# Performance work log

Hardware: AMD Instinct MI355X
Metric: run time of the kernel (lower is better)

The kernel has to match this reference:

```python
import jax, jax.numpy as jnp
import numpy as np


def setup_inputs() -> dict:
    key = jax.random.key(0)
    ks = jax.random.split(key, 8)
    B, H, W, C = 4, 64, 64, 256
    Ck = C // 8  # key/query channels
    x = jax.random.normal(ks[0], (B, H, W, C), dtype=jnp.float32)
    Wf = jax.random.normal(ks[1], (C, Ck), dtype=jnp.float32) * (1.0 / np.sqrt(C))
    Wg = jax.random.normal(ks[2], (C, Ck), dtype=jnp.float32) * (1.0 / np.sqrt(C))
    Wh = jax.random.normal(ks[3], (C, C), dtype=jnp.float32) * (1.0 / np.sqrt(C))
    bf = jnp.zeros((Ck,), dtype=jnp.float32)
    bg = jnp.zeros((Ck,), dtype=jnp.float32)
    bh = jnp.zeros((C,), dtype=jnp.float32)
    gamma = jax.random.normal(ks[4], (), dtype=jnp.float32) * 0.1
    return {"x": x, "Wf": Wf, "bf": bf, "Wg": Wg, "bg": bg, "Wh": Wh, "bh": bh, "gamma": gamma}


def reference(x, Wf, bf, Wg, bg, Wh, bh, gamma):
    B, H, W, C = x.shape
    N = H * W
    # 1x1 convs == per-pixel matmuls over channel dim
    f = jnp.einsum('bhwc,ck->bhwk', x, Wf) + bf  # [B,H,W,C/8]
    g = jnp.einsum('bhwc,ck->bhwk', x, Wg) + bg  # [B,H,W,C/8]
    h = jnp.einsum('bhwc,cd->bhwd', x, Wh) + bh  # [B,H,W,C]
    f_flat = f.reshape(B, N, -1)
    g_flat = g.reshape(B, N, -1)
    h_flat = h.reshape(B, N, C)
    # s[b,i,j] = <g_i, f_j>   (query = g, key = f, as in the TF code)
    s = jnp.einsum('bik,bjk->bij', g_flat, f_flat)  # [B,N,N]
    b = jax.nn.softmax(s, axis=-1)
    o = jnp.einsum('bij,bjd->bid', b, h_flat)  # [B,N,C]
    y = gamma * o.reshape(B, H, W, C) + x
    return y
```

## Files before the change

### kernel.cpp

```cpp
#include <hip/hip_runtime.h>
#include <hip/hip_bf16.h>
#include <math.h>


typedef __bf16 bf16x8 __attribute__((ext_vector_type(8)));
typedef __bf16 bf16x4 __attribute__((ext_vector_type(4)));
typedef float f32x4 __attribute__((ext_vector_type(4)));

#define NPIX 4096
#define CDIM 256
#define CK   32

__device__ __forceinline__ void gload_lds16(const void* g, void* l) {
    __builtin_amdgcn_global_load_lds(
        (const __attribute__((address_space(1))) unsigned int*)g,
        (__attribute__((address_space(3))) unsigned int*)l, 16, 0, 0);
}

__global__ __launch_bounds__(256) void prep_wtf(
    const float* __restrict__ Wf, const float* __restrict__ Wg,
    const float* __restrict__ Wh, __bf16* __restrict__ WTf)
{
    const int ct = blockIdx.x;
    for (int i = threadIdx.x; i < 16 * 256; i += 256) {
        const int l15 = i >> 8;
        const int k = i & 255;
        const int c = ct * 16 + l15;
        float v;
        if (c < 32)      v = Wf[k * 32 + c];
        else if (c < 64) v = Wg[k * 32 + (c - 32)];
        else             v = Wh[k * 256 + (c - 64)];
        WTf[((size_t)(ct * 8 + (k >> 5)) * 16 + l15) * 32 + (k & 31)] = (__bf16)v;
    }
}

__global__ __launch_bounds__(256, 4) void proj_mfma(
    const float* __restrict__ x, const __bf16* __restrict__ WTf,
    const float* __restrict__ bf_, const float* __restrict__ bg_,
    const float* __restrict__ bh_,
    __bf16* __restrict__ fbuf, __bf16* __restrict__ gbuf,
    __bf16* __restrict__ hT)
{
    __shared__ __bf16 xs[16 * 256];

    const int t = threadIdx.x;
    const int rowbase = blockIdx.x * 16;

    #pragma unroll
    for (int i = 0; i < 4; ++i) {
        const int flat = i * 1024 + t * 4;
        const int row = flat >> 8, col = flat & 255;
        const float4 xv = *(const float4*)&x[(size_t)rowbase * 256 + flat];
        const int sc = col ^ ((row & 7) << 3);
        *(bf16x4*)&xs[row * 256 + sc] =
            (bf16x4){(__bf16)xv.x, (__bf16)xv.y, (__bf16)xv.z, (__bf16)xv.w};
    }
    __syncthreads();

    const int wv = t >> 6, lane = t & 63, l15 = lane & 15, lhi = lane >> 4;

    const f32x4 zero4 = {0.f, 0.f, 0.f, 0.f};
    f32x4 acc[5];
    #pragma unroll
    for (int i = 0; i < 5; ++i) acc[i] = zero4;

    for (int kk = 0; kk < 8; ++kk) {
        const int col = (kk * 32 + lhi * 8) ^ ((l15 & 7) << 3);
        const bf16x8 xfrag = *(const bf16x8*)&xs[l15 * 256 + col];
        if (wv == 0) {
            #pragma unroll
            for (int i = 0; i < 4; ++i) {
                const bf16x8 w = *(const bf16x8*)&WTf[((size_t)(i * 8 + kk) * 16 + l15) * 32 + lhi * 8];
                acc[i] = __builtin_amdgcn_mfma_f32_16x16x32_bf16(xfrag, w, acc[i], 0, 0, 0);
            }
            const bf16x8 w = *(const bf16x8*)&WTf[((size_t)(4 * 8 + kk) * 16 + l15) * 32 + lhi * 8];
            acc[4] = __builtin_amdgcn_mfma_f32_16x16x32_bf16(w, xfrag, acc[4], 0, 0, 0);
        } else {
            #pragma unroll
            for (int i = 0; i < 5; ++i) {
                const int ctg = 4 + (wv - 1) * 5 + i + 1;
                const bf16x8 w = *(const bf16x8*)&WTf[((size_t)(ctg * 8 + kk) * 16 + l15) * 32 + lhi * 8];
                acc[i] = __builtin_amdgcn_mfma_f32_16x16x32_bf16(w, xfrag, acc[i], 0, 0, 0);
            }
        }
    }

    const int b = rowbase >> 12;
    const int n = (rowbase & 4095) + l15;
    if (wv == 0) {
        #pragma unroll
        for (int i = 0; i < 2; ++i) {
            const float bia = bf_[i * 16 + l15];
            #pragma unroll
            for (int r = 0; r < 4; ++r)
                fbuf[(size_t)(rowbase + lhi * 4 + r) * CK + i * 16 + l15] =
                    (__bf16)(acc[i][r] + bia);
        }
        #pragma unroll
        for (int i = 0; i < 2; ++i) {
            const float bia = bg_[i * 16 + l15];
            #pragma unroll
            for (int r = 0; r < 4; ++r)
                gbuf[(size_t)(rowbase + lhi * 4 + r) * CK + i * 16 + l15] =
                    (__bf16)(acc[i + 2][r] + bia);
        }
        #pragma unroll
        for (int r = 0; r < 4; ++r) {
            const int d = lhi * 4 + r;
            hT[((size_t)b * CDIM + d) * NPIX + n] = (__bf16)(acc[4][r] + bh_[d]);
        }
    } else {
        #pragma unroll
        for (int i = 0; i < 5; ++i) {
            const int dt = (wv - 1) * 5 + i + 1;
            #pragma unroll
            for (int r = 0; r < 4; ++r) {
                const int d = dt * 16 + lhi * 4 + r;
                hT[((size_t)b * CDIM + d) * NPIX + n] = (__bf16)(acc[i][r] + bh_[d]);
            }
        }
    }
}

#define ATTN_BODY(T, HU, HL)                                                        \
{                                                                                   \
    const int cb_ = (T) & 1;                                                        \
    if (wv < 4) {                                                                   \
        const f32x4 m30 = {-30.f, -30.f, -30.f, -30.f};                             \
        f32x4 s[4];                                                                 \
        _Pragma("unroll")                                                           \
        for (int cb = 0; cb < 4; ++cb) {                                            \
            const int r = cb * 16 + l15;                                            \
            const bf16x8 fr = *(const bf16x8*)                                      \
                &fs[cb_][r][(lhi ^ (r & 3) ^ ((r >> 2) & 3)) * 8];                  \
            s[cb] = __builtin_amdgcn_mfma_f32_16x16x32_bf16(ga, fr, m30, 0, 0, 0);  \
        }                                                                           \
        _Pragma("unroll")                                                           \
        for (int cb = 0; cb < 4; ++cb) {                                            \
            _Pragma("unroll")                                                       \
            for (int r = 0; r < 4; ++r) {                                           \
                const float p = __expf(s[cb][r]);                                   \
                lsum[r] += p;                                                       \
                pbuf[cb_][wv * 16 + lhi * 4 + r][cb * 16 + l15] = (__bf16)p;        \
            }                                                                       \
        }                                                                           \
        if ((T) < 63)                                                               \
            gload_lds16(fsrc_ + (size_t)((T) + 1) * 64 * CK,                        \
                        &fs[cb_ ^ 1][wv * 16][0]);                                  \
    }                                                                               \
    __syncthreads();                                                                \
    if ((T) < 63) {                                                                 \
        const size_t kvn = (size_t)((T) + 1) * 64;                                  \
        _Pragma("unroll")                                                           \
        for (int dt = 0; dt < 2; ++dt)                                              \
            _Pragma("unroll")                                                       \
            for (int kh = 0; kh < 2; ++kh)                                          \
                HL[dt * 2 + kh] = *(const bf16x8*)                                  \
                    (hp + (size_t)dt * 16 * NPIX + kvn + kh * 32);                  \
    }                                                                               \
    __builtin_amdgcn_s_setprio(1);                                                  \
    _Pragma("unroll")                                                               \
    for (int rt = 0; rt < 4; ++rt) {                                                \
        const bf16x8 pa0 = *(const bf16x8*)&pbuf[cb_][rt * 16 + l15][lhi * 8];      \
        const bf16x8 pa1 = *(const bf16x8*)&pbuf[cb_][rt * 16 + l15][32 + lhi * 8]; \
        _Pragma("unroll")                                                           \
        for (int dt = 0; dt < 2; ++dt) {                                            \
            O_[rt][dt] = __builtin_amdgcn_mfma_f32_16x16x32_bf16(                   \
                pa0, HU[dt * 2 + 0], O_[rt][dt], 0, 0, 0);                          \
            O_[rt][dt] = __builtin_amdgcn_mfma_f32_16x16x32_bf16(                   \
                pa1, HU[dt * 2 + 1], O_[rt][dt], 0, 0, 0);                          \
        }                                                                           \
    }                                                                               \
    __builtin_amdgcn_s_setprio(0);                                                  \
}

__global__ __launch_bounds__(512, 2) void attn_kernel(
    const __bf16* __restrict__ fbuf, const __bf16* __restrict__ gbuf,
    const __bf16* __restrict__ hT, const float* __restrict__ x,
    const float* __restrict__ gamma_p, float* __restrict__ out)
{
    __shared__ __bf16 pbuf[2][64][72];
    __shared__ __bf16 fs[2][64][32];
    __shared__ float lbuf[64];

    const int t = threadIdx.x;
    const int lane = t & 63;
    const int wv = t >> 6;
    const int l15 = lane & 15;
    const int lhi = lane >> 4;

    const int xcd = blockIdx.x & 7;
    const int b = xcd >> 1;
    const int qt = ((blockIdx.x >> 3) << 1) + (xcd & 1);
    const int q0 = qt * 64;

    const __bf16* hb = hT + (size_t)b * CDIM * NPIX;
    const __bf16* fbp = fbuf + (size_t)b * NPIX * CK;

    const __bf16* hp = hb + (size_t)(wv * 32 + l15) * NPIX + lhi * 8;

    bf16x8 ga = {};
    if (wv < 4)
        ga = *(const bf16x8*)&gbuf[((size_t)b * NPIX + q0 + wv * 16 + l15) * CK + lhi * 8];
    const int frow = lane >> 2;
    const __bf16* fsrc_ = fbp + (size_t)(wv * 16 + frow) * CK
                              + ((lane & 3) ^ (frow & 3) ^ ((frow >> 2) & 3)) * 8;

    const f32x4 zero4 = {0.f, 0.f, 0.f, 0.f};
    f32x4 O_[4][2];
    #pragma unroll
    for (int i = 0; i < 4; ++i) { O_[i][0] = zero4; O_[i][1] = zero4; }
    float lsum[4] = {0.f, 0.f, 0.f, 0.f};

    bf16x8 hA[4], hB[4];

    if (wv < 4) gload_lds16(fsrc_, &fs[0][wv * 16][0]);
    #pragma unroll
    for (int dt = 0; dt < 2; ++dt)
        #pragma unroll
        for (int kh = 0; kh < 2; ++kh)
            hA[dt * 2 + kh] = *(const bf16x8*)(hp + (size_t)dt * 16 * NPIX + kh * 32);
    __syncthreads();

    for (int it = 0; it < 32; ++it) {
        ATTN_BODY(2 * it,     hA, hB);
        ATTN_BODY(2 * it + 1, hB, hA);
    }

    if (wv < 4) {
        #pragma unroll
        for (int r = 0; r < 4; ++r) {
            lsum[r] += __shfl_xor(lsum[r], 1, 64);
            lsum[r] += __shfl_xor(lsum[r], 2, 64);
            lsum[r] += __shfl_xor(lsum[r], 4, 64);
            lsum[r] += __shfl_xor(lsum[r], 8, 64);
        }
        if (l15 == 0) {
            #pragma unroll
            for (int r = 0; r < 4; ++r)
                lbuf[wv * 16 + lhi * 4 + r] = lsum[r];
        }
    }
    __syncthreads();

    const float gm = gamma_p[0];
    #pragma unroll
    for (int rt = 0; rt < 4; ++rt) {
        #pragma unroll
        for (int rr = 0; rr < 4; ++rr) {
            const int row = rt * 16 + lhi * 4 + rr;
            const float rl = gm / lbuf[row];
            const size_t base = ((size_t)b * NPIX + q0 + row) * CDIM + wv * 32;
            #pragma unroll
            for (int dt = 0; dt < 2; ++dt) {
                const size_t idx = base + dt * 16 + l15;
                out[idx] = fmaf(rl, O_[rt][dt][rr], x[idx]);
            }
        }
    }
}

extern "C" void kernel_launch(void* const* d_in, const int* in_sizes, int n_in,
                              void* d_out, int out_size, void* d_ws, size_t ws_size,
                              hipStream_t stream)
{
    const float* x     = (const float*)d_in[0];
    const float* Wf    = (const float*)d_in[1];
    const float* bf    = (const float*)d_in[2];
    const float* Wg    = (const float*)d_in[3];
    const float* bg    = (const float*)d_in[4];
    const float* Wh    = (const float*)d_in[5];
    const float* bh    = (const float*)d_in[6];
    const float* gamma = (const float*)d_in[7];
    float* out = (float*)d_out;

    __bf16* fbuf = (__bf16*)d_ws;
    __bf16* gbuf = fbuf + (size_t)4 * NPIX * CK;
    __bf16* hT   = gbuf + (size_t)4 * NPIX * CK;
    __bf16* WTf  = hT + (size_t)4 * CDIM * NPIX;

    prep_wtf<<<20, 256, 0, stream>>>(Wf, Wg, Wh, WTf);
    proj_mfma<<<1024, 256, 0, stream>>>(x, WTf, bf, bg, bh, fbuf, gbuf, hT);
    attn_kernel<<<256, 512, 0, stream>>>(fbuf, gbuf, hT, x, gamma, out);
}
```

Baseline: 178.2 us.

## Rework projection tiling and attention kernel with register-held K and permlane P packing

The projection kernel now handles 64 rows per 512-thread block, with a split of waves between the f/g and h outputs so weight fragments are reused across row blocks. It also uses packed bf16 conversion. The attention kernel drops the LDS staging of f and loads K fragments straight into double-buffered registers. Softmax probabilities are packed with permlane swaps into a compact LDS layout, and the PV work is rebalanced so the four score waves take fewer output columns. prep_wtf is also parallelized over more blocks. This aims to cut LDS traffic and barrier stalls and to balance work across waves, at the cost of higher register pressure and a 1-block occupancy bound.

```diff
diff --git a/kernel.cpp b/kernel.cpp
--- a/kernel.cpp
+++ b/kernel.cpp
@@ -4,183 +4,222 @@
 
 
 typedef __bf16 bf16x8 __attribute__((ext_vector_type(8)));
-typedef __bf16 bf16x4 __attribute__((ext_vector_type(4)));
 typedef float f32x4 __attribute__((ext_vector_type(4)));
 
 #define NPIX 4096
 #define CDIM 256
 #define CK   32
 
-__device__ __forceinline__ void gload_lds16(const void* g, void* l) {
-    __builtin_amdgcn_global_load_lds(
-        (const __attribute__((address_space(1))) unsigned int*)g,
-        (__attribute__((address_space(3))) unsigned int*)l, 16, 0, 0);
+union U128 { unsigned int d[4]; uint4 u4; bf16x8 v; };
+
+__device__ __forceinline__ unsigned int cvtpk(float lo, float hi) {
+    unsigned int r;
+    asm("v_cvt_pk_bf16_f32 %0, %1, %2" : "=v"(r) : "v"(lo), "v"(hi));
+    return r;
 }
 
 __global__ __launch_bounds__(256) void prep_wtf(
     const float* __restrict__ Wf, const float* __restrict__ Wg,
     const float* __restrict__ Wh, __bf16* __restrict__ WTf)
 {
-    const int ct = blockIdx.x;
-    for (int i = threadIdx.x; i < 16 * 256; i += 256) {
-        const int l15 = i >> 8;
-        const int k = i & 255;
-        const int c = ct * 16 + l15;
-        float v;
-        if (c < 32)      v = Wf[k * 32 + c];
-        else if (c < 64) v = Wg[k * 32 + (c - 32)];
-        else             v = Wh[k * 256 + (c - 64)];
-        WTf[((size_t)(ct * 8 + (k >> 5)) * 16 + l15) * 32 + (k & 31)] = (__bf16)v;
-    }
-}
-
-__global__ __launch_bounds__(256, 4) void proj_mfma(
+    const int k = blockIdx.x;
+    const int c = threadIdx.x;
+    const int kk = k >> 5, kj = k & 31;
+    {
+        const float v = Wh[k * 256 + c];
+        const int ct = 4 + (c >> 4), l15 = c & 15;
+        WTf[((size_t)(ct * 8 + kk) * 16 + l15) * 32 + kj] = (__bf16)v;
+    }
+    if (c < 32) {
+        const float v = Wf[k * 32 + c];
+        const int ct = c >> 4, l15 = c & 15;
+        WTf[((size_t)(ct * 8 + kk) * 16 + l15) * 32 + kj] = (__bf16)v;
+    } else if (c < 64) {
+        const int cc = c - 32;
+        const float v = Wg[k * 32 + cc];
+        const int ct = 2 + (cc >> 4), l15 = cc & 15;
+        WTf[((size_t)(ct * 8 + kk) * 16 + l15) * 32 + kj] = (__bf16)v;
+    }
+}
+
+__global__ __launch_bounds__(512, 1) void proj_mfma(
     const float* __restrict__ x, const __bf16* __restrict__ WTf,
     const float* __restrict__ bf_, const float* __restrict__ bg_,
     const float* __restrict__ bh_,
     __bf16* __restrict__ fbuf, __bf16* __restrict__ gbuf,
     __bf16* __restrict__ hT)
 {
-    __shared__ __bf16 xs[16 * 256];
+    __shared__ __bf16 xs[64 * 256];
 
     const int t = threadIdx.x;
-    const int rowbase = blockIdx.x * 16;
+    const int rowbase = blockIdx.x * 64;
 
     #pragma unroll
-    for (int i = 0; i < 4; ++i) {
-        const int flat = i * 1024 + t * 4;
+    for (int i = 0; i < 8; ++i) {
+        const int flat = i * 2048 + t * 4;
         const int row = flat >> 8, col = flat & 255;
         const float4 xv = *(const float4*)&x[(size_t)rowbase * 256 + flat];
-        const int sc = col ^ ((row & 7) << 3);
-        *(bf16x4*)&xs[row * 256 + sc] =
-            (bf16x4){(__bf16)xv.x, (__bf16)xv.y, (__bf16)xv.z, (__bf16)xv.w};
+        const unsigned int d0 = cvtpk(xv.x, xv.y);
+        const unsigned int d1 = cvtpk(xv.z, xv.w);
+        const int s = (col >> 3) ^ (row & 7);
+        uint2 w; w.x = d0; w.y = d1;
+        *(uint2*)&xs[row * 256 + s * 8 + (col & 7)] = w;
     }
     __syncthreads();
 
     const int wv = t >> 6, lane = t & 63, l15 = lane & 15, lhi = lane >> 4;
-
-    const f32x4 zero4 = {0.f, 0.f, 0.f, 0.f};
-    f32x4 acc[5];
-    #pragma unroll
-    for (int i = 0; i < 5; ++i) acc[i] = zero4;
-
-    for (int kk = 0; kk < 8; ++kk) {
-        const int col = (kk * 32 + lhi * 8) ^ ((l15 & 7) << 3);
-        const bf16x8 xfrag = *(const bf16x8*)&xs[l15 * 256 + col];
-        if (wv == 0) {
-            #pragma unroll
-            for (int i = 0; i < 4; ++i) {
-                const bf16x8 w = *(const bf16x8*)&WTf[((size_t)(i * 8 + kk) * 16 + l15) * 32 + lhi * 8];
-                acc[i] = __builtin_amdgcn_mfma_f32_16x16x32_bf16(xfrag, w, acc[i], 0, 0, 0);
-            }
-            const bf16x8 w = *(const bf16x8*)&WTf[((size_t)(4 * 8 + kk) * 16 + l15) * 32 + lhi * 8];
-            acc[4] = __builtin_amdgcn_mfma_f32_16x16x32_bf16(w, xfrag, acc[4], 0, 0, 0);
-        } else {
-            #pragma unroll
-            for (int i = 0; i < 5; ++i) {
-                const int ctg = 4 + (wv - 1) * 5 + i + 1;
-                const bf16x8 w = *(const bf16x8*)&WTf[((size_t)(ctg * 8 + kk) * 16 + l15) * 32 + lhi * 8];
-                acc[i] = __builtin_amdgcn_mfma_f32_16x16x32_bf16(w, xfrag, acc[i], 0, 0, 0);
-            }
-        }
-    }
-
     const int b = rowbase >> 12;
-    const int n = (rowbase & 4095) + l15;
-    if (wv == 0) {
-        #pragma unroll
-        for (int i = 0; i < 2; ++i) {
-            const float bia = bf_[i * 16 + l15];
-            #pragma unroll
-            for (int r = 0; r < 4; ++r)
-                fbuf[(size_t)(rowbase + lhi * 4 + r) * CK + i * 16 + l15] =
-                    (__bf16)(acc[i][r] + bia);
-        }
-        #pragma unroll
-        for (int i = 0; i < 2; ++i) {
-            const float bia = bg_[i * 16 + l15];
-            #pragma unroll
-            for (int r = 0; r < 4; ++r)
-                gbuf[(size_t)(rowbase + lhi * 4 + r) * CK + i * 16 + l15] =
-                    (__bf16)(acc[i + 2][r] + bia);
-        }
-        #pragma unroll
-        for (int r = 0; r < 4; ++r) {
-            const int d = lhi * 4 + r;
-            hT[((size_t)b * CDIM + d) * NPIX + n] = (__bf16)(acc[4][r] + bh_[d]);
+    const int nloc = rowbase & 4095;
+
+    if (wv < 2) {
+        const int rb0 = wv * 2;
+        f32x4 acc[4][2];
+        #pragma unroll
+        for (int c = 0; c < 4; ++c)
+            #pragma unroll
+            for (int rb = 0; rb < 2; ++rb) acc[c][rb] = (f32x4){0.f, 0.f, 0.f, 0.f};
+        #pragma unroll
+        for (int kk = 0; kk < 8; ++kk) {
+            bf16x8 xf[2];
+            #pragma unroll
+            for (int rb = 0; rb < 2; ++rb) {
+                const int row = (rb0 + rb) * 16 + l15;
+                xf[rb] = *(const bf16x8*)&xs[row * 256 + (((kk * 4 + lhi) ^ (row & 7)) * 8)];
+            }
+            #pragma unroll
+            for (int c = 0; c < 4; ++c) {
+                const bf16x8 w = *(const bf16x8*)&WTf[((size_t)(c * 8 + kk) * 16 + l15) * 32 + lhi * 8];
+                acc[c][0] = __builtin_amdgcn_mfma_f32_16x16x32_bf16(xf[0], w, acc[c][0], 0, 0, 0);
+                acc[c][1] = __builtin_amdgcn_mfma_f32_16x16x32_bf16(xf[1], w, acc[c][1], 0, 0, 0);
+            }
+        }
+        #pragma unroll
+        for (int c = 0; c < 4; ++c) {
+            const float bia = (c < 2) ? bf_[c * 16 + l15] : bg_[(c - 2) * 16 + l15];
+            __bf16* dst = (c < 2) ? fbuf : gbuf;
+            const int ch = (c & 1) * 16 + l15;
+            #pragma unroll
+            for (int rb = 0; rb < 2; ++rb)
+                #pragma unroll
+                for (int r = 0; r < 4; ++r)
+                    dst[(size_t)(rowbase + (rb0 + rb) * 16 + lhi * 4 + r) * CK + ch] =
+                        (__bf16)(acc[c][rb][r] + bia);
         }
     } else {
-        #pragma unroll
-        for (int i = 0; i < 5; ++i) {
-            const int dt = (wv - 1) * 5 + i + 1;
-            #pragma unroll
-            for (int r = 0; r < 4; ++r) {
-                const int d = dt * 16 + lhi * 4 + r;
-                hT[((size_t)b * CDIM + d) * NPIX + n] = (__bf16)(acc[i][r] + bh_[d]);
-            }
-        }
-    }
-}
-
-#define ATTN_BODY(T, HU, HL)                                                        \
-{                                                                                   \
-    const int cb_ = (T) & 1;                                                        \
+        const int nct = (wv < 6) ? 3 : 2;
+        const int ct0 = (wv < 6) ? (wv - 2) * 3 : 12 + (wv - 6) * 2;
+        f32x4 acc[3][4];
+        #pragma unroll
+        for (int c = 0; c < 3; ++c)
+            #pragma unroll
+            for (int rb = 0; rb < 4; ++rb) acc[c][rb] = (f32x4){0.f, 0.f, 0.f, 0.f};
+        #pragma unroll
+        for (int kk = 0; kk < 8; ++kk) {
+            bf16x8 xf[4];
+            #pragma unroll
+            for (int rb = 0; rb < 4; ++rb) {
+                const int row = rb * 16 + l15;
+                xf[rb] = *(const bf16x8*)&xs[row * 256 + (((kk * 4 + lhi) ^ (row & 7)) * 8)];
+            }
+            #pragma unroll
+            for (int c = 0; c < 3; ++c) {
+                if (c < nct) {
+                    const bf16x8 w = *(const bf16x8*)
+                        &WTf[((size_t)((4 + ct0 + c) * 8 + kk) * 16 + l15) * 32 + lhi * 8];
+                    #pragma unroll
+                    for (int rb = 0; rb < 4; ++rb)
+                        acc[c][rb] = __builtin_amdgcn_mfma_f32_16x16x32_bf16(w, xf[rb], acc[c][rb], 0, 0, 0);
+                }
+            }
+        }
+        #pragma unroll
+        for (int c = 0; c < 3; ++c) {
+            if (c < nct) {
+                #pragma unroll
+                for (int r = 0; r < 4; ++r) {
+                    const int ch = (ct0 + c) * 16 + lhi * 4 + r;
+                    const float bia = bh_[ch];
+                    #pragma unroll
+                    for (int rb = 0; rb < 4; ++rb)
+                        hT[((size_t)b * CDIM + ch) * NPIX + nloc + rb * 16 + l15] =
+                            (__bf16)(acc[c][rb][r] + bia);
+                }
+            }
+        }
+    }
+}
+
+#define PL32(a, b) asm("v_permlane32_swap_b32 %0, %1" : "+v"(a), "+v"(b))
+#define PL16(a, b) asm("v_permlane16_swap_b32 %0, %1" : "+v"(a), "+v"(b))
+
+#define ATTN_TILE(KV, PB, FC, FN, HC, HN)                                           \
+do {                                                                                \
     if (wv < 4) {                                                                   \
         const f32x4 m30 = {-30.f, -30.f, -30.f, -30.f};                             \
-        f32x4 s[4];                                                                 \
-        _Pragma("unroll")                                                           \
-        for (int cb = 0; cb < 4; ++cb) {                                            \
-            const int r = cb * 16 + l15;                                            \
-            const bf16x8 fr = *(const bf16x8*)                                      \
-                &fs[cb_][r][(lhi ^ (r & 3) ^ ((r >> 2) & 3)) * 8];                  \
-            s[cb] = __builtin_amdgcn_mfma_f32_16x16x32_bf16(ga, fr, m30, 0, 0, 0);  \
+        f32x4 s0 = __builtin_amdgcn_mfma_f32_16x16x32_bf16(FC[0], ga, m30, 0, 0, 0);\
+        f32x4 s1 = __builtin_amdgcn_mfma_f32_16x16x32_bf16(FC[1], ga, m30, 0, 0, 0);\
+        f32x4 s2 = __builtin_amdgcn_mfma_f32_16x16x32_bf16(FC[2], ga, m30, 0, 0, 0);\
+        f32x4 s3 = __builtin_amdgcn_mfma_f32_16x16x32_bf16(FC[3], ga, m30, 0, 0, 0);\
+        {                                                 \
+            const size_t ko = (size_t)((KV) + 64) * CK;                             \
+            FN[0] = *(const bf16x8*)(fp + ko);                                      \
+            FN[1] = *(const bf16x8*)(fp + ko + 16 * CK);                            \
+            FN[2] = *(const bf16x8*)(fp + ko + 32 * CK);                            \
+            FN[3] = *(const bf16x8*)(fp + ko + 48 * CK);                            \
         }                                                                           \
-        _Pragma("unroll")                                                           \
-        for (int cb = 0; cb < 4; ++cb) {                                            \
-            _Pragma("unroll")                                                       \
-            for (int r = 0; r < 4; ++r) {                                           \
-                const float p = __expf(s[cb][r]);                                   \
-                lsum[r] += p;                                                       \
-                pbuf[cb_][wv * 16 + lhi * 4 + r][cb * 16 + l15] = (__bf16)p;        \
-            }                                                                       \
-        }                                                                           \
-        if ((T) < 63)                                                               \
-            gload_lds16(fsrc_ + (size_t)((T) + 1) * 64 * CK,                        \
-                        &fs[cb_ ^ 1][wv * 16][0]);                                  \
+        float p0 = __expf(s0[0]), p1 = __expf(s0[1]), p2 = __expf(s0[2]), p3 = __expf(s0[3]); \
+        float p4 = __expf(s1[0]), p5 = __expf(s1[1]), p6 = __expf(s1[2]), p7 = __expf(s1[3]); \
+        float p8 = __expf(s2[0]), p9 = __expf(s2[1]), pa_ = __expf(s2[2]), pb_ = __expf(s2[3]); \
+        float pc_ = __expf(s3[0]), pd_ = __expf(s3[1]), pe_ = __expf(s3[2]), pf_ = __expf(s3[3]); \
+        lsum += ((p0 + p1) + (p2 + p3)) + ((p4 + p5) + (p6 + p7))                   \
+              + ((p8 + p9) + (pa_ + pb_)) + ((pc_ + pd_) + (pe_ + pf_));            \
+        unsigned int u0 = cvtpk(p0, p1), u1 = cvtpk(p2, p3);                        \
+        unsigned int u2 = cvtpk(p4, p5), u3 = cvtpk(p6, p7);                        \
+        unsigned int u4 = cvtpk(p8, p9), u5 = cvtpk(pa_, pb_);                      \
+        unsigned int u6 = cvtpk(pc_, pd_), u7 = cvtpk(pe_, pf_);                    \
+        PL32(u0, u2); PL32(u1, u3); PL32(u4, u6); PL32(u5, u7);                     \
+        PL16(u0, u2); PL16(u1, u3); PL16(u4, u6); PL16(u5, u7);                     \
+        uint4 w0; w0.x = u0; w0.y = u1; w0.z = u2; w0.w = u3;                       \
+        uint4 w1; w1.x = u4; w1.y = u5; w1.z = u6; w1.w = u7;                       \
+        pbuf[PB][wv * 2 + 0][lane] = w0;                                            \
+        pbuf[PB][wv * 2 + 1][lane] = w1;                                            \
     }                                                                               \
     __syncthreads();                                                                \
-    if ((T) < 63) {                                                                 \
-        const size_t kvn = (size_t)((T) + 1) * 64;                                  \
-        _Pragma("unroll")                                                           \
-        for (int dt = 0; dt < 2; ++dt)                                              \
-            _Pragma("unroll")                                                       \
-            for (int kh = 0; kh < 2; ++kh)                                          \
-                HL[dt * 2 + kh] = *(const bf16x8*)                                  \
-                    (hp + (size_t)dt * 16 * NPIX + kvn + kh * 32);                  \
+    {                                                     \
+        const size_t kn = (size_t)((KV) + 64);                                      \
+        HN[0] = *(const bf16x8*)(hp + kn);                                          \
+        HN[1] = *(const bf16x8*)(hp + kn + 32);                                     \
+        if (wv >= 4) {                                                              \
+            HN[2] = *(const bf16x8*)(hp + (size_t)16 * NPIX + kn);                  \
+            HN[3] = *(const bf16x8*)(hp + (size_t)16 * NPIX + kn + 32);             \
+            HN[4] = *(const bf16x8*)(hp + (size_t)32 * NPIX + kn);                  \
+            HN[5] = *(const bf16x8*)(hp + (size_t)32 * NPIX + kn + 32);             \
+        }                                                                           \
     }                                                                               \
     __builtin_amdgcn_s_setprio(1);                                                  \
     _Pragma("unroll")                                                               \
     for (int rt = 0; rt < 4; ++rt) {                                                \
-        const bf16x8 pa0 = *(const bf16x8*)&pbuf[cb_][rt * 16 + l15][lhi * 8];      \
-        const bf16x8 pa1 = *(const bf16x8*)&pbuf[cb_][rt * 16 + l15][32 + lhi * 8]; \
-        _Pragma("unroll")                                                           \
-        for (int dt = 0; dt < 2; ++dt) {                                            \
-            O_[rt][dt] = __builtin_amdgcn_mfma_f32_16x16x32_bf16(                   \
-                pa0, HU[dt * 2 + 0], O_[rt][dt], 0, 0, 0);                          \
-            O_[rt][dt] = __builtin_amdgcn_mfma_f32_16x16x32_bf16(                   \
-                pa1, HU[dt * 2 + 1], O_[rt][dt], 0, 0, 0);                          \
+        U128 A0, A1;                                                                \
+        A0.u4 = pbuf[PB][rt * 2 + 0][lane];                                         \
+        A1.u4 = pbuf[PB][rt * 2 + 1][lane];                                         \
+        O_[rt][0] = __builtin_amdgcn_mfma_f32_16x16x32_bf16(A0.v, HC[0], O_[rt][0], 0, 0, 0); \
+        O_[rt][0] = __builtin_amdgcn_mfma_f32_16x16x32_bf16(A1.v, HC[1], O_[rt][0], 0, 0, 0); \
+        if (wv >= 4) {                                                              \
+            O_[rt][1] = __builtin_amdgcn_mfma_f32_16x16x32_bf16(A0.v, HC[2], O_[rt][1], 0, 0, 0); \
+            O_[rt][1] = __builtin_amdgcn_mfma_f32_16x16x32_bf16(A1.v, HC[3], O_[rt][1], 0, 0, 0); \
+            O_[rt][2] = __builtin_amdgcn_mfma_f32_16x16x32_bf16(A0.v, HC[4], O_[rt][2], 0, 0, 0); \
+            O_[rt][2] = __builtin_amdgcn_mfma_f32_16x16x32_bf16(A1.v, HC[5], O_[rt][2], 0, 0, 0); \
         }                                                                           \
     }                                                                               \
     __builtin_amdgcn_s_setprio(0);                                                  \
-}
-
-__global__ __launch_bounds__(512, 2) void attn_kernel(
+} while (0)
+
+__global__ __launch_bounds__(512, 1) void attn_kernel(
     const __bf16* __restrict__ fbuf, const __bf16* __restrict__ gbuf,
     const __bf16* __restrict__ hT, const float* __restrict__ x,
     const float* __restrict__ gamma_p, float* __restrict__ out)
 {
-    __shared__ __bf16 pbuf[2][64][72];
-    __shared__ __bf16 fs[2][64][32];
+    __shared__ uint4 pbuf[2][8][64];
     __shared__ float lbuf[64];
 
     const int t = threadIdx.x;
@@ -194,52 +233,51 @@
     const int qt = ((blockIdx.x >> 3) << 1) + (xcd & 1);
     const int q0 = qt * 64;
 
+    const __bf16* fb = fbuf + (size_t)b * NPIX * CK;
     const __bf16* hb = hT + (size_t)b * CDIM * NPIX;
-    const __bf16* fbp = fbuf + (size_t)b * NPIX * CK;
-
-    const __bf16* hp = hb + (size_t)(wv * 32 + l15) * NPIX + lhi * 8;
+
+    const int dbase = (wv < 4) ? wv * 16 : 64 + (wv - 4) * 48;
+    const __bf16* hp = hb + (size_t)(dbase + l15) * NPIX + lhi * 8;
+    const __bf16* fp = fb + (size_t)l15 * CK + lhi * 8;
 
     bf16x8 ga = {};
     if (wv < 4)
         ga = *(const bf16x8*)&gbuf[((size_t)b * NPIX + q0 + wv * 16 + l15) * CK + lhi * 8];
-    const int frow = lane >> 2;
-    const __bf16* fsrc_ = fbp + (size_t)(wv * 16 + frow) * CK
-                              + ((lane & 3) ^ (frow & 3) ^ ((frow >> 2) & 3)) * 8;
-
-    const f32x4 zero4 = {0.f, 0.f, 0.f, 0.f};
-    f32x4 O_[4][2];
+
+    f32x4 O_[4][3];
     #pragma unroll
-    for (int i = 0; i < 4; ++i) { O_[i][0] = zero4; O_[i][1] = zero4; }
-    float lsum[4] = {0.f, 0.f, 0.f, 0.f};
-
-    bf16x8 hA[4], hB[4];
-
-    if (wv < 4) gload_lds16(fsrc_, &fs[0][wv * 16][0]);
-    #pragma unroll
-    for (int dt = 0; dt < 2; ++dt)
-        #pragma unroll
-        for (int kh = 0; kh < 2; ++kh)
-            hA[dt * 2 + kh] = *(const bf16x8*)(hp + (size_t)dt * 16 * NPIX + kh * 32);
-    __syncthreads();
+    for (int i = 0; i < 4; ++i)
+        #pragma unroll
+        for (int j = 0; j < 3; ++j) O_[i][j] = (f32x4){0.f, 0.f, 0.f, 0.f};
+    float lsum = 0.f;
+
+    bf16x8 FA[4], FB[4], HA[6], HB[6];
+
+    if (wv < 4) {
+        FA[0] = *(const bf16x8*)(fp);
+        FA[1] = *(const bf16x8*)(fp + 16 * CK);
+        FA[2] = *(const bf16x8*)(fp + 32 * CK);
+        FA[3] = *(const bf16x8*)(fp + 48 * CK);
+    }
+    HA[0] = *(const bf16x8*)(hp);
+    HA[1] = *(const bf16x8*)(hp + 32);
+    if (wv >= 4) {
+        HA[2] = *(const bf16x8*)(hp + (size_t)16 * NPIX);
+        HA[3] = *(const bf16x8*)(hp + (size_t)16 * NPIX + 32);
+        HA[4] = *(const bf16x8*)(hp + (size_t)32 * NPIX);
+        HA[5] = *(const bf16x8*)(hp + (size_t)32 * NPIX + 32);
+    }
 
     for (int it = 0; it < 32; ++it) {
-        ATTN_BODY(2 * it,     hA, hB);
-        ATTN_BODY(2 * it + 1, hB, hA);
+        const int kv = it * 128;
+        ATTN_TILE(kv,      0, FA, FB, HA, HB);
+        ATTN_TILE(kv + 64, 1, FB, FA, HB, HA);
     }
 
     if (wv < 4) {
-        #pragma unroll
-        for (int r = 0; r < 4; ++r) {
-            lsum[r] += __shfl_xor(lsum[r], 1, 64);
-            lsum[r] += __shfl_xor(lsum[r], 2, 64);
-            lsum[r] += __shfl_xor(lsum[r], 4, 64);
-            lsum[r] += __shfl_xor(lsum[r], 8, 64);
-        }
-        if (l15 == 0) {
-            #pragma unroll
-            for (int r = 0; r < 4; ++r)
-                lbuf[wv * 16 + lhi * 4 + r] = lsum[r];
-        }
+        lsum += __shfl_xor(lsum, 16, 64);
+        lsum += __shfl_xor(lsum, 32, 64);
+        if (lane < 16) lbuf[wv * 16 + l15] = lsum;
     }
     __syncthreads();
 
@@ -247,14 +285,14 @@
     #pragma unroll
     for (int rt = 0; rt < 4; ++rt) {
         #pragma unroll
-        for (int rr = 0; rr < 4; ++rr) {
-            const int row = rt * 16 + lhi * 4 + rr;
+        for (int r = 0; r < 4; ++r) {
+            const int row = rt * 16 + lhi * 4 + r;
             const float rl = gm / lbuf[row];
-            const size_t base = ((size_t)b * NPIX + q0 + row) * CDIM + wv * 32;
-            #pragma unroll
-            for (int dt = 0; dt < 2; ++dt) {
-                const size_t idx = base + dt * 16 + l15;
-                out[idx] = fmaf(rl, O_[rt][dt][rr], x[idx]);
+            const size_t base = ((size_t)b * NPIX + q0 + row) * CDIM + dbase;
+            out[base + l15] = fmaf(rl, O_[rt][0][r], x[base + l15]);
+            if (wv >= 4) {
+                out[base + 16 + l15] = fmaf(rl, O_[rt][1][r], x[base + 16 + l15]);
+                out[base + 32 + l15] = fmaf(rl, O_[rt][2][r], x[base + 32 + l15]);
             }
         }
     }
@@ -279,7 +317,7 @@
     __bf16* hT   = gbuf + (size_t)4 * NPIX * CK;
     __bf16* WTf  = hT + (size_t)4 * CDIM * NPIX;
 
-    prep_wtf<<<20, 256, 0, stream>>>(Wf, Wg, Wh, WTf);
-    proj_mfma<<<1024, 256, 0, stream>>>(x, WTf, bf, bg, bh, fbuf, gbuf, hT);
+    prep_wtf<<<256, 256, 0, stream>>>(Wf, Wg, Wh, WTf);
+    proj_mfma<<<256, 512, 0, stream>>>(x, WTf, bf, bg, bh, fbuf, gbuf, hT);
     attn_kernel<<<256, 512, 0, stream>>>(fbuf, gbuf, hT, x, gamma, out);
 }
```

Result: slower. 182.3 us (+2.3%).
